# Optimization experiments

Hardware: AMD Instinct MI355X
Metric: run time of the kernel (lower is better)

The kernel has to match this reference:

```python
import jax, jax.numpy as jnp
import numpy as np
from jax import lax

BATCH = 8192
PATCH = 2
STRIDE = 2
OUT_CH = 4
NUM_PATCHES = ((28 - PATCH) // STRIDE + 1) ** 2  # 196
THRESHOLD = 0.8
EPS = 1e-12


def setup_inputs() -> dict:
    key = jax.random.key(0)
    k1, k2, k3, k4, k5 = jax.random.split(key, 5)
    x = jax.random.normal(k1, (BATCH, 1, 28, 28), dtype=jnp.float32)
    conv_w = jax.random.normal(k2, (OUT_CH, 1, PATCH, PATCH), dtype=jnp.float32) * 0.5
    conv_b = jax.random.normal(k3, (OUT_CH,), dtype=jnp.float32) * 0.1
    feat_dim = OUT_CH * NUM_PATCHES + NUM_PATCHES  # 784 + 196 = 980
    lin_w = jax.random.normal(k4, (10, feat_dim), dtype=jnp.float32) * 0.02
    lin_b = jax.random.normal(k5, (10,), dtype=jnp.float32) * 0.01
    return {"x": x, "conv_w": conv_w, "conv_b": conv_b, "lin_w": lin_w, "lin_b": lin_b}


def reference(x, conv_w, conv_b, lin_w, lin_b):
    # conv patch embed: (B,1,28,28) -> (B,C,14,14)
    f = lax.conv_general_dilated(
        x, conv_w, window_strides=(STRIDE, STRIDE), padding="VALID",
        dimension_numbers=("NCHW", "OIHW", "NCHW"))
    f = f + conv_b[None, :, None, None]
    B = f.shape[0]
    flat = f.reshape(B, -1)  # (B, C*P) channel-major, matches torch .view
    # replicate feat.view(num_patches, -1): rows of length C from the flat vector
    pf = flat.reshape(B, NUM_PATCHES, -1)  # (B, P, C)
    nrm = pf / (jnp.linalg.norm(pf, axis=-1, keepdims=True) + EPS)
    # squared cosine similarity = state fidelity, all pairs at once
    fid = jnp.einsum("bpc,bqc->bpq", nrm, nrm) ** 2  # (B, P, P)
    w = (fid >= THRESHOLD).astype(flat.dtype)
    w = w * (1.0 - jnp.eye(NUM_PATCHES, dtype=flat.dtype))  # no self-edges
    deg = jnp.sum(w, axis=-1)  # weighted degree per node, (B, P)
    feats = jnp.concatenate([flat, deg], axis=1)  # (B, 980)
    logits = feats @ lin_w.T + lin_b
    return jax.nn.log_softmax(logits, axis=-1)
```

## Files before the change

### kernel.cpp

```cpp
#include <hip/hip_runtime.h>
#include <math.h>


#define NP 196
#define FEAT 980
#define COS_TH 0.894427190999915878f

typedef short v4s  __attribute__((ext_vector_type(4)));
typedef short v8s  __attribute__((ext_vector_type(8)));
typedef float v16f __attribute__((ext_vector_type(16)));

static __device__ __forceinline__ float bf2f(short s) {
    return __uint_as_float(((uint32_t)(uint16_t)s) << 16);
}

__global__ __launch_bounds__(256, 7) void quanv_kernel(
    const float* __restrict__ x,
    const float* __restrict__ conv_w,
    const float* __restrict__ conv_b,
    const float* __restrict__ lin_w,
    const float* __restrict__ lin_b,
    float* __restrict__ out)
{
    __shared__ __align__(16) float s_x[2][784];
    __shared__ __align__(16) short s_P[2][256][8];
    __shared__ __align__(16) float s_feats[2][FEAT];

    int*   s_deg    = (int*)s_x;
    int*   s_cred   = s_deg + 384;
    float* s_part   = (float*)(s_cred + 392);
    float* s_logits = s_part + 500;

    const int b = blockIdx.x;
    const int t = threadIdx.x;
    const int w = t >> 6, l = t & 63;

    if (t < NP) {
        ((float4*)s_x[0])[t] = ((const float4*)(x + (size_t)(2 * b)     * 784))[t];
        ((float4*)s_x[1])[t] = ((const float4*)(x + (size_t)(2 * b + 1) * 784))[t];
    }
    __syncthreads();

    if (t < NP) {
        int h = t / 14, ww = t - 14 * (t / 14);
        #pragma unroll
        for (int img = 0; img < 2; ++img) {
            const float* r0 = s_x[img] + (2 * h) * 28 + 2 * ww;
            float x00 = r0[0], x01 = r0[1], x10 = r0[28], x11 = r0[29];
            #pragma unroll
            for (int c = 0; c < 4; ++c) {
                float f = conv_b[c]
                        + conv_w[c * 4 + 0] * x00 + conv_w[c * 4 + 1] * x01
                        + conv_w[c * 4 + 2] * x10 + conv_w[c * 4 + 3] * x11;
                s_feats[img][c * NP + t] = f;
            }
        }
    }
    __syncthreads();

    {
        #pragma unroll
        for (int img = 0; img < 2; ++img) {
            v8s pk = {0, 0, 0, 0, 0, 0, 0, 0};
            if (t < NP) {
                float4 v = ((const float4*)s_feats[img])[t];
                float n = sqrtf(v.x * v.x + v.y * v.y + v.z * v.z + v.w * v.w);
                float inv = 1.0f / (n + 1e-12f);
                float e[4] = { v.x * inv, v.y * inv, v.z * inv, v.w * inv };
                #pragma unroll
                for (int k = 0; k < 4; ++k) {
                    uint32_t bx = __float_as_uint(e[k]);
                    uint32_t rh = bx + 0x7FFFu + ((bx >> 16) & 1u);
                    uint32_t hk = rh >> 16;
                    float hif = __uint_as_float(hk << 16);
                    float res = e[k] - hif;
                    uint32_t br = __float_as_uint(res);
                    uint32_t rl = br + 0x7FFFu + ((br >> 16) & 1u);
                    pk[k]     = (short)hk;
                    pk[4 + k] = (short)(rl >> 16);
                }
            }
            *(v8s*)&s_P[img][t][0] = pk;
        }
        if (t < NP) { s_cred[t] = 0; s_cred[196 + t] = 0; }
    }
    __syncthreads();

    v16f zacc = {0.f,0.f,0.f,0.f,0.f,0.f,0.f,0.f,
                 0.f,0.f,0.f,0.f,0.f,0.f,0.f,0.f};
    asm("" : "+v"(zacc));

    const int ln = l & 31, half = l >> 5;

    #pragma unroll
    for (int jj = 0; jj < 3; ++jj) {
        const int job = w + 4 * jj;
        const int img = (job >= 6) ? 1 : 0;
        const int j = job - 6 * img;
        const short* Pbase = &s_P[img][0][0];

        v4s bh = *(const v4s*)(Pbase + (32 * j + ln) * 8 + 4 * half);
        v8s B = __builtin_shufflevector(bh, bh, 0, 1, 2, 3, 0, 1, 2, 3);

        unsigned c0 = 0u, c1 = 0u;
        #pragma unroll
        for (int i = 0; i < 6; ++i) {
            v8s A = *(const v8s*)(Pbase + (32 * i + ln) * 8);
            v16f acc = __builtin_amdgcn_mfma_f32_32x32x16_bf16(A, B, zacc, 0, 0, 0);
            #pragma unroll
            for (int e = 0; e < 16; e += 2) {
                c0 += (fabsf(acc[e])     >= COS_TH) ? 1u : 0u;
                c1 += (fabsf(acc[e + 1]) >= COS_TH) ? 1u : 0u;
            }
        }
        unsigned cnt = c0 + c1;
        cnt += __shfl_down(cnt, 32, 64);
        if (l < 32)
            s_deg[img * 192 + 32 * j + l] = (int)cnt;
    }

    #pragma unroll
    for (int img = 0; img < 2; ++img) {
        const int r = 192 + w;
        const short* pr = &s_P[img][r][0];
        float pe0 = bf2f(pr[0]) + bf2f(pr[4]);
        float pe1 = bf2f(pr[1]) + bf2f(pr[5]);
        float pe2 = bf2f(pr[2]) + bf2f(pr[6]);
        float pe3 = bf2f(pr[3]) + bf2f(pr[7]);
        unsigned total = 0u;
        #pragma unroll
        for (int k = 0; k < 4; ++k) {
            int q = 64 * k + l;
            const short* qr = &s_P[img][q][0];
            float d =          pe0 * (bf2f(qr[0]) + bf2f(qr[4]));
            d = fmaf(pe1, bf2f(qr[1]) + bf2f(qr[5]), d);
            d = fmaf(pe2, bf2f(qr[2]) + bf2f(qr[6]), d);
            d = fmaf(pe3, bf2f(qr[3]) + bf2f(qr[7]), d);
            bool hit = fabsf(d) >= COS_TH;
            unsigned long long m = __ballot(hit);
            total += (unsigned)__popcll(m);
            if (hit && q < 192)
                atomicAdd(&s_cred[img * 196 + q], 1);
        }
        if (l == 0)
            s_feats[img][784 + r] = (float)(int)total - 1.0f;
    }
    __syncthreads();

    if (t < 192) {
        s_feats[0][784 + t] = (float)(s_deg[t]       + s_cred[t])       - 1.0f;
        s_feats[1][784 + t] = (float)(s_deg[192 + t] + s_cred[196 + t]) - 1.0f;
    }
    __syncthreads();

    if (t < 250) {
        int k = t / 25, c = t - 25 * (t / 25);
        const float4* wrow = (const float4*)(lin_w + k * FEAT);
        const float4* f0p = (const float4*)s_feats[0];
        const float4* f1p = (const float4*)s_feats[1];
        float a0 = 0.0f, a1 = 0.0f;
        for (int i = c; i < 245; i += 25) {
            float4 wv = wrow[i];
            float4 f0 = f0p[i];
            float4 f1 = f1p[i];
            a0 = fmaf(f0.x, wv.x, a0); a1 = fmaf(f1.x, wv.x, a1);
            a0 = fmaf(f0.y, wv.y, a0); a1 = fmaf(f1.y, wv.y, a1);
            a0 = fmaf(f0.z, wv.z, a0); a1 = fmaf(f1.z, wv.z, a1);
            a0 = fmaf(f0.w, wv.w, a0); a1 = fmaf(f1.w, wv.w, a1);
        }
        s_part[t]       = a0;
        s_part[250 + t] = a1;
    }
    __syncthreads();

    if (t < 20) {
        int img = t / 10, k = t - 10 * (t / 10);
        const float* part = s_part + 250 * img;
        float s = lin_b[k];
        #pragma unroll
        for (int i = 0; i < 25; ++i) s += part[k * 25 + i];
        s_logits[10 * img + k] = s;
    }
    __syncthreads();

    if (t < 20) {
        int img = t / 10, k = t - 10 * (t / 10);
        const float* lg = s_logits + 10 * img;
        float m = -INFINITY;
        #pragma unroll
        for (int j2 = 0; j2 < 10; ++j2) m = fmaxf(m, lg[j2]);
        float s = 0.0f;
        #pragma unroll
        for (int j2 = 0; j2 < 10; ++j2) s += expf(lg[j2] - m);
        out[(size_t)(2 * b + img) * 10 + k] = lg[k] - m - logf(s);
    }
}

extern "C" void kernel_launch(void* const* d_in, const int* in_sizes, int n_in,
                              void* d_out, int out_size, void* d_ws, size_t ws_size,
                              hipStream_t stream) {
    const float* x      = (const float*)d_in[0];
    const float* conv_w = (const float*)d_in[1];
    const float* conv_b = (const float*)d_in[2];
    const float* lin_w  = (const float*)d_in[3];
    const float* lin_b  = (const float*)d_in[4];
    float* out = (float*)d_out;
    quanv_kernel<<<dim3(4096), dim3(256), 0, stream>>>(x, conv_w, conv_b, lin_w, lin_b, out);
}
```

Baseline: 104.6 us.

## Process one image per block and split MFMA row tiles across waves

```diff
diff --git a/kernel.cpp b/kernel.cpp
--- a/kernel.cpp
+++ b/kernel.cpp
@@ -14,7 +14,7 @@
     return __uint_as_float(((uint32_t)(uint16_t)s) << 16);
 }
 
-__global__ __launch_bounds__(256, 7) void quanv_kernel(
+__global__ __launch_bounds__(256, 8) void quanv_kernel(
     const float* __restrict__ x,
     const float* __restrict__ conv_w,
     const float* __restrict__ conv_b,
@@ -22,67 +22,59 @@
     const float* __restrict__ lin_b,
     float* __restrict__ out)
 {
-    __shared__ __align__(16) float s_x[2][784];
-    __shared__ __align__(16) short s_P[2][256][8];
-    __shared__ __align__(16) float s_feats[2][FEAT];
-
-    int*   s_deg    = (int*)s_x;
-    int*   s_cred   = s_deg + 384;
-    float* s_part   = (float*)(s_cred + 392);
-    float* s_logits = s_part + 500;
+    __shared__ __align__(16) float s_x[784];
+    __shared__ __align__(16) short s_P[256][8];
+    __shared__ __align__(16) float s_feats[FEAT];
+    __shared__ __align__(16) int   s_deg0[192];
+    __shared__ __align__(16) int   s_deg1[192];
+    __shared__ __align__(16) int   s_cred[196];
+    __shared__ __align__(16) float s_part[250];
+    __shared__ __align__(16) float s_logits[10];
 
     const int b = blockIdx.x;
     const int t = threadIdx.x;
     const int w = t >> 6, l = t & 63;
 
-    if (t < NP) {
-        ((float4*)s_x[0])[t] = ((const float4*)(x + (size_t)(2 * b)     * 784))[t];
-        ((float4*)s_x[1])[t] = ((const float4*)(x + (size_t)(2 * b + 1) * 784))[t];
-    }
+    if (t < NP)
+        ((float4*)s_x)[t] = ((const float4*)(x + (size_t)b * 784))[t];
     __syncthreads();
 
     if (t < NP) {
         int h = t / 14, ww = t - 14 * (t / 14);
+        const float* r0 = s_x + (2 * h) * 28 + 2 * ww;
+        float x00 = r0[0], x01 = r0[1], x10 = r0[28], x11 = r0[29];
         #pragma unroll
-        for (int img = 0; img < 2; ++img) {
-            const float* r0 = s_x[img] + (2 * h) * 28 + 2 * ww;
-            float x00 = r0[0], x01 = r0[1], x10 = r0[28], x11 = r0[29];
-            #pragma unroll
-            for (int c = 0; c < 4; ++c) {
-                float f = conv_b[c]
-                        + conv_w[c * 4 + 0] * x00 + conv_w[c * 4 + 1] * x01
-                        + conv_w[c * 4 + 2] * x10 + conv_w[c * 4 + 3] * x11;
-                s_feats[img][c * NP + t] = f;
-            }
+        for (int c = 0; c < 4; ++c) {
+            float f = conv_b[c]
+                    + conv_w[c * 4 + 0] * x00 + conv_w[c * 4 + 1] * x01
+                    + conv_w[c * 4 + 2] * x10 + conv_w[c * 4 + 3] * x11;
+            s_feats[c * NP + t] = f;
         }
     }
     __syncthreads();
 
     {
-        #pragma unroll
-        for (int img = 0; img < 2; ++img) {
-            v8s pk = {0, 0, 0, 0, 0, 0, 0, 0};
-            if (t < NP) {
-                float4 v = ((const float4*)s_feats[img])[t];
-                float n = sqrtf(v.x * v.x + v.y * v.y + v.z * v.z + v.w * v.w);
-                float inv = 1.0f / (n + 1e-12f);
-                float e[4] = { v.x * inv, v.y * inv, v.z * inv, v.w * inv };
-                #pragma unroll
-                for (int k = 0; k < 4; ++k) {
-                    uint32_t bx = __float_as_uint(e[k]);
-                    uint32_t rh = bx + 0x7FFFu + ((bx >> 16) & 1u);
-                    uint32_t hk = rh >> 16;
-                    float hif = __uint_as_float(hk << 16);
-                    float res = e[k] - hif;
-                    uint32_t br = __float_as_uint(res);
-                    uint32_t rl = br + 0x7FFFu + ((br >> 16) & 1u);
-                    pk[k]     = (short)hk;
-                    pk[4 + k] = (short)(rl >> 16);
-                }
+        v8s pk = {0, 0, 0, 0, 0, 0, 0, 0};
+        if (t < NP) {
+            float4 v = ((const float4*)s_feats)[t];
+            float n = sqrtf(v.x * v.x + v.y * v.y + v.z * v.z + v.w * v.w);
+            float inv = 1.0f / (n + 1e-12f);
+            float e[4] = { v.x * inv, v.y * inv, v.z * inv, v.w * inv };
+            #pragma unroll
+            for (int k = 0; k < 4; ++k) {
+                uint32_t bx = __float_as_uint(e[k]);
+                uint32_t rh = bx + 0x7FFFu + ((bx >> 16) & 1u);
+                uint32_t hk = rh >> 16;
+                float hif = __uint_as_float(hk << 16);
+                float res = e[k] - hif;
+                uint32_t br = __float_as_uint(res);
+                uint32_t rl = br + 0x7FFFu + ((br >> 16) & 1u);
+                pk[k]     = (short)hk;
+                pk[4 + k] = (short)(rl >> 16);
             }
-            *(v8s*)&s_P[img][t][0] = pk;
         }
-        if (t < NP) { s_cred[t] = 0; s_cred[196 + t] = 0; }
+        *(v8s*)&s_P[t][0] = pk;
+        if (t < NP) s_cred[t] = 0;
     }
     __syncthreads();
 
@@ -95,16 +87,17 @@
     #pragma unroll
     for (int jj = 0; jj < 3; ++jj) {
         const int job = w + 4 * jj;
-        const int img = (job >= 6) ? 1 : 0;
-        const int j = job - 6 * img;
-        const short* Pbase = &s_P[img][0][0];
+        const int j = job >> 1;
+        const int h = job & 1;
+        const short* Pbase = &s_P[0][0];
 
         v4s bh = *(const v4s*)(Pbase + (32 * j + ln) * 8 + 4 * half);
         v8s B = __builtin_shufflevector(bh, bh, 0, 1, 2, 3, 0, 1, 2, 3);
 
         unsigned c0 = 0u, c1 = 0u;
         #pragma unroll
-        for (int i = 0; i < 6; ++i) {
+        for (int ii = 0; ii < 3; ++ii) {
+            const int i = 3 * h + ii;
             v8s A = *(const v8s*)(Pbase + (32 * i + ln) * 8);
             v16f acc = __builtin_amdgcn_mfma_f32_32x32x16_bf16(A, B, zacc, 0, 0, 0);
             #pragma unroll
@@ -115,14 +108,15 @@
         }
         unsigned cnt = c0 + c1;
         cnt += __shfl_down(cnt, 32, 64);
-        if (l < 32)
-            s_deg[img * 192 + 32 * j + l] = (int)cnt;
+        if (l < 32) {
+            int* dst = h ? s_deg1 : s_deg0;
+            dst[32 * j + l] = (int)cnt;
+        }
     }
 
-    #pragma unroll
-    for (int img = 0; img < 2; ++img) {
+    {
         const int r = 192 + w;
-        const short* pr = &s_P[img][r][0];
+        const short* pr = &s_P[r][0];
         float pe0 = bf2f(pr[0]) + bf2f(pr[4]);
         float pe1 = bf2f(pr[1]) + bf2f(pr[5]);
         float pe2 = bf2f(pr[2]) + bf2f(pr[6]);
@@ -131,7 +125,7 @@
         #pragma unroll
         for (int k = 0; k < 4; ++k) {
             int q = 64 * k + l;
-            const short* qr = &s_P[img][q][0];
+            const short* qr = &s_P[q][0];
             float d =          pe0 * (bf2f(qr[0]) + bf2f(qr[4]));
             d = fmaf(pe1, bf2f(qr[1]) + bf2f(qr[5]), d);
             d = fmaf(pe2, bf2f(qr[2]) + bf2f(qr[6]), d);
@@ -140,59 +134,50 @@
             unsigned long long m = __ballot(hit);
             total += (unsigned)__popcll(m);
             if (hit && q < 192)
-                atomicAdd(&s_cred[img * 196 + q], 1);
+                atomicAdd(&s_cred[q], 1);
         }
         if (l == 0)
-            s_feats[img][784 + r] = (float)(int)total - 1.0f;
+            s_feats[784 + r] = (float)(int)total - 1.0f;
     }
     __syncthreads();
 
-    if (t < 192) {
-        s_feats[0][784 + t] = (float)(s_deg[t]       + s_cred[t])       - 1.0f;
-        s_feats[1][784 + t] = (float)(s_deg[192 + t] + s_cred[196 + t]) - 1.0f;
-    }
+    if (t < 192)
+        s_feats[784 + t] = (float)(s_deg0[t] + s_deg1[t] + s_cred[t]) - 1.0f;
     __syncthreads();
 
     if (t < 250) {
         int k = t / 25, c = t - 25 * (t / 25);
         const float4* wrow = (const float4*)(lin_w + k * FEAT);
-        const float4* f0p = (const float4*)s_feats[0];
-        const float4* f1p = (const float4*)s_feats[1];
-        float a0 = 0.0f, a1 = 0.0f;
+        const float4* fp = (const float4*)s_feats;
+        float a0 = 0.0f;
         for (int i = c; i < 245; i += 25) {
             float4 wv = wrow[i];
-            float4 f0 = f0p[i];
-            float4 f1 = f1p[i];
-            a0 = fmaf(f0.x, wv.x, a0); a1 = fmaf(f1.x, wv.x, a1);
-            a0 = fmaf(f0.y, wv.y, a0); a1 = fmaf(f1.y, wv.y, a1);
-            a0 = fmaf(f0.z, wv.z, a0); a1 = fmaf(f1.z, wv.z, a1);
-            a0 = fmaf(f0.w, wv.w, a0); a1 = fmaf(f1.w, wv.w, a1);
+            float4 f0 = fp[i];
+            a0 = fmaf(f0.x, wv.x, a0);
+            a0 = fmaf(f0.y, wv.y, a0);
+            a0 = fmaf(f0.z, wv.z, a0);
+            a0 = fmaf(f0.w, wv.w, a0);
         }
-        s_part[t]       = a0;
-        s_part[250 + t] = a1;
+        s_part[t] = a0;
     }
     __syncthreads();
 
-    if (t < 20) {
-        int img = t / 10, k = t - 10 * (t / 10);
-        const float* part = s_part + 250 * img;
-        float s = lin_b[k];
+    if (t < 10) {
+        float s = lin_b[t];
         #pragma unroll
-        for (int i = 0; i < 25; ++i) s += part[k * 25 + i];
-        s_logits[10 * img + k] = s;
+        for (int i = 0; i < 25; ++i) s += s_part[t * 25 + i];
+        s_logits[t] = s;
     }
     __syncthreads();
 
-    if (t < 20) {
-        int img = t / 10, k = t - 10 * (t / 10);
-        const float* lg = s_logits + 10 * img;
+    if (t < 10) {
         float m = -INFINITY;
         #pragma unroll
-        for (int j2 = 0; j2 < 10; ++j2) m = fmaxf(m, lg[j2]);
+        for (int j2 = 0; j2 < 10; ++j2) m = fmaxf(m, s_logits[j2]);
         float s = 0.0f;
         #pragma unroll
-        for (int j2 = 0; j2 < 10; ++j2) s += expf(lg[j2] - m);
-        out[(size_t)(2 * b + img) * 10 + k] = lg[k] - m - logf(s);
+        for (int j2 = 0; j2 < 10; ++j2) s += expf(s_logits[j2] - m);
+        out[(size_t)b * 10 + t] = s_logits[t] - m - logf(s);
     }
 }
 
@@ -205,5 +190,5 @@
     const float* lin_w  = (const float*)d_in[3];
     const float* lin_b  = (const float*)d_in[4];
     float* out = (float*)d_out;
-    quanv_kernel<<<dim3(4096), dim3(256), 0, stream>>>(x, conv_w, conv_b, lin_w, lin_b, out);
+    quanv_kernel<<<dim3(8192), dim3(256), 0, stream>>>(x, conv_w, conv_b, lin_w, lin_b, out);
 }
```

Measured after the change: 106.6 us. No clear change (+1.9%).
